# Optimization experiments

Hardware: AMD Instinct MI355X
Metric: run time of the kernel (lower is better)

## Reference

```python
import jax, jax.numpy as jnp
import numpy as np

DIM = 128
HEADS = 4
HEAD_DIM = DIM // HEADS
WIN = 7
DIL = 1
EPS = 1e-5
HIDDEN = 4 * DIM  # mlp_ratio = 4.0
PAD = DIL * (WIN // 2)


def setup_inputs() -> dict:
    key = jax.random.key(0)
    ks = jax.random.split(key, 16)
    s = 0.02
    return {
        "x": jax.random.normal(ks[0], (8, DIM, 256, 256), dtype=jnp.float32),
        "n1_w": jnp.ones((DIM,), jnp.float32),
        "n1_b": jnp.zeros((DIM,), jnp.float32),
        "qkv_w": jax.random.normal(ks[1], (3 * DIM, DIM), jnp.float32) * s,
        "qkv_b": jnp.zeros((3 * DIM,), jnp.float32),
        "proj_w": jax.random.normal(ks[2], (DIM, DIM), jnp.float32) * s,
        "proj_b": jnp.zeros((DIM,), jnp.float32),
        "n2_w": jnp.ones((DIM,), jnp.float32),
        "n2_b": jnp.zeros((DIM,), jnp.float32),
        "mlp_w1": jax.random.normal(ks[3], (HIDDEN, DIM), jnp.float32) * s,
        "mlp_b1": jnp.zeros((HIDDEN,), jnp.float32),
        "mlp_w2": jax.random.normal(ks[4], (DIM, HIDDEN), jnp.float32) * s,
        "mlp_b2": jnp.zeros((DIM,), jnp.float32),
    }


def _channel_ln(x, w, b):
    # LayerNorm over channel axis (axis=1) of NCHW, per spatial location
    mu = jnp.mean(x, axis=1, keepdims=True)
    var = jnp.mean(jnp.square(x - mu), axis=1, keepdims=True)
    xn = (x - mu) * jax.lax.rsqrt(var + EPS)
    return xn * w[None, :, None, None] + b[None, :, None, None]


def _local_attn(x, qkv_w, qkv_b, proj_w, proj_b):
    B, C, H, W = x.shape
    qkv = jnp.einsum("oc,bchw->bohw", qkv_w, x) + qkv_b[None, :, None, None]
    q, k, v = jnp.split(qkv, 3, axis=1)
    q = q.reshape(B, HEADS, HEAD_DIM, H, W) * (HEAD_DIM ** -0.5)
    k = k.reshape(B, HEADS, HEAD_DIM, H, W)
    v = v.reshape(B, HEADS, HEAD_DIM, H, W)
    # boundary_pad='zeros': pad key/value maps with zeros
    pad = [(0, 0), (0, 0), (0, 0), (PAD, PAD), (PAD, PAD)]
    kp = jnp.pad(k, pad)
    vp = jnp.pad(v, pad)
    offsets = [(oi, oj) for oi in range(WIN) for oj in range(WIN)]
    scores = []
    for oi, oj in offsets:  # fixed small window loop (49 iters)
        ks = kp[..., oi * DIL : oi * DIL + H, oj * DIL : oj * DIL + W]
        scores.append(jnp.einsum("bhcij,bhcij->bhij", q, ks))
    scores = jnp.stack(scores, axis=-1)
    attn = jax.nn.softmax(scores, axis=-1)
    out = jnp.zeros_like(v)
    for idx, (oi, oj) in enumerate(offsets):
        vs = vp[..., oi * DIL : oi * DIL + H, oj * DIL : oj * DIL + W]
        out = out + attn[..., idx][:, :, None] * vs
    out = out.reshape(B, C, H, W)
    return jnp.einsum("oc,bchw->bohw", proj_w, out) + proj_b[None, :, None, None]


def _mlp(x, w1, b1, w2, b2):
    h = jnp.einsum("oc,bchw->bohw", w1, x) + b1[None, :, None, None]
    h = jax.nn.gelu(h)
    return jnp.einsum("oc,bchw->bohw", w2, h) + b2[None, :, None, None]


def reference(x, n1_w, n1_b, qkv_w, qkv_b, proj_w, proj_b, n2_w, n2_b, mlp_w1, mlp_b1, mlp_w2, mlp_b2):
    x = x + _local_attn(_channel_ln(x, n1_w, n1_b), qkv_w, qkv_b, proj_w, proj_b)
    x = x + _mlp(_channel_ln(x, n2_w, n2_b), mlp_w1, mlp_b1, mlp_w2, mlp_b2)
    return x
```

## Files before the change

kernel.cpp:

```cpp
#include <hip/hip_runtime.h>
#include <hip/hip_bf16.h>

typedef unsigned short u16;
typedef unsigned int u32;
typedef __attribute__((ext_vector_type(4))) u32 u32x4;
typedef __attribute__((ext_vector_type(2))) u32 u32x2;
typedef __attribute__((ext_vector_type(8))) __bf16 bf16x8;
typedef __attribute__((ext_vector_type(4))) float f32x4;
typedef __attribute__((ext_vector_type(4))) short short4v;

#define HW 65536
#define MFMA32(a, b, c) __builtin_amdgcn_mfma_f32_16x16x32_bf16((a), (b), (c), 0, 0, 0)

__device__ __forceinline__ u16 f2bf(float f){
  union { u32 i; float f; } v; v.f = f;
  u32 r = v.i + 0x7fffu + ((v.i >> 16) & 1u);
  return (u16)(r >> 16);
}
__device__ __forceinline__ u32 pkbf(float a, float b){
  __bf16 lo = (__bf16)a, hi = (__bf16)b;
  u16 ulo = __builtin_bit_cast(u16, lo);
  u16 uhi = __builtin_bit_cast(u16, hi);
  return (u32)ulo | ((u32)uhi << 16);
}
__device__ __forceinline__ float rcpf(float x){
#if __has_builtin(__builtin_amdgcn_rcpf)
  return __builtin_amdgcn_rcpf(x);
#else
  return 1.0f / x;
#endif
}
__device__ __forceinline__ float gelu_tanh(float v){
  float t = v * v;
  float u = fmaf(0.044715f * t, v, v);
  float z = 1.5957691216057308f * u;
  float e = __expf(-z);
  return v * rcpf(1.0f + e);
}

__device__ __forceinline__ f32x4 mfma16bf16(short4v a, short4v b, f32x4 c){
#if __has_builtin(__builtin_amdgcn_mfma_f32_16x16x16bf16_1k)
  return __builtin_amdgcn_mfma_f32_16x16x16bf16_1k(a, b, c, 0, 0, 0);
#else
  f32x4 d;
  asm volatile("v_mfma_f32_16x16x16_bf16 %0, %1, %2, %3"
               : "=v"(d) : "v"(a), "v"(b), "v"(c));
  return d;
#endif
}

__global__ __launch_bounds__(256) void k_pack(
    const float* __restrict__ qkvw, const float* __restrict__ projw,
    const float* __restrict__ w1, const float* __restrict__ w2,
    u16* __restrict__ wf)
{
  int tile = blockIdx.x;
  int t = threadIdx.x;
  int l = t >> 1, half = t & 1;
  if (l >= 64) return;
  int lg = l >> 4;
  if (tile >= 256){
    int ti = tile - 256;
    int hp = ti >> 3, m = ti & 7;
    int row = m * 16 + (l & 15);
    u16 o[4];
    #pragma unroll
    for (int j = 0; j < 4; ++j){
      int s = half * 4 + j;
      int kloc = (s < 4) ? (4 * lg + s) : (16 + 4 * lg + (s - 4));
      o[j] = f2bf(w2[(size_t)row * 512 + hp * 32 + kloc]);
    }
    u32x2 v; v[0] = (u32)o[0] | ((u32)o[1] << 16); v[1] = (u32)o[2] | ((u32)o[3] << 16);
    *(u32x2*)(wf + 131072 + ti * 512 + l * 8 + half * 4) = v;
    return;
  }
  const float* W; int base, ti;
  if (tile < 96)       { W = qkvw; base = 0;     ti = tile; }
  else if (tile < 128) { W = projw; base = 49152; ti = tile - 96; }
  else                 { W = w1;   base = 65536; ti = tile - 128; }
  int mt = ti / 4, kt = ti % 4;
  int r0 = half * 4;
  int m = mt * 16 + (l & 15);
  int kb = kt * 32 + 8 * lg + r0;
  u16 o[4];
  #pragma unroll
  for (int j = 0; j < 4; ++j) o[j] = f2bf(W[(size_t)m * 128 + kb + j]);
  u32x2 v; v[0] = (u32)o[0] | ((u32)o[1] << 16); v[1] = (u32)o[2] | ((u32)o[3] << 16);
  *(u32x2*)(wf + base + ti * 512 + l * 8 + r0) = v;
}

__global__ __launch_bounds__(256, 2) void k_ln_qkv(
    const float* __restrict__ x, const float* __restrict__ n1w,
    const float* __restrict__ n1b, const u16* __restrict__ wfq,
    const float* __restrict__ qkvb, u16* __restrict__ qkvp)
{
  __shared__ __align__(16) char smem[66560];
  float* red  = (float*)(smem + 16384);
  float* mu_s = (float*)(smem + 18432);
  float* rs_s = (float*)(smem + 18688);

  const int t = threadIdx.x;
  const int w = t >> 6, l = t & 63;
  const int P0 = blockIdx.x * 64;
  const int b = P0 >> 16;
  const int pix0 = P0 & 65535;
  const float* xb = x + ((size_t)b * 128) * HW + pix0 + l;

  float xv[32];
  float s = 0.f, s2 = 0.f;
  #pragma unroll
  for (int j = 0; j < 32; ++j){
    float v = xb[(size_t)(w * 32 + j) * HW];
    xv[j] = v; s += v; s2 += v * v;
  }
  red[w * 64 + l] = s;
  red[256 + w * 64 + l] = s2;
  __syncthreads();
  if (t < 64){
    float ss  = red[t] + red[64 + t] + red[128 + t] + red[192 + t];
    float ss2 = red[256 + t] + red[320 + t] + red[384 + t] + red[448 + t];
    float mu = ss * 0.0078125f;
    float var = ss2 * 0.0078125f - mu * mu;
    mu_s[t] = mu; rs_s[t] = rsqrtf(var + 1e-5f);
  }
  __syncthreads();
  {
    float mu = mu_s[l], rs = rs_s[l];
    #pragma unroll
    for (int jj = 0; jj < 4; ++jj){
      int c0 = w * 32 + jj * 8;
      u32x4 pk;
      #pragma unroll
      for (int k2 = 0; k2 < 4; ++k2){
        float v0 = (xv[jj*8 + k2*2    ] - mu) * rs * n1w[c0 + k2*2    ] + n1b[c0 + k2*2    ];
        float v1 = (xv[jj*8 + k2*2 + 1] - mu) * rs * n1w[c0 + k2*2 + 1] + n1b[c0 + k2*2 + 1];
        pk[k2] = pkbf(v0, v1);
      }
      *(u32x4*)(smem + l * 256 + (((w * 4 + jj) ^ (l & 7)) << 4)) = pk;
    }
  }
  __syncthreads();

  const int lg = l >> 4, ln = l & 15;
  const bf16x8* wfrag = (const bf16x8*)wfq;
  f32x4 acc[6][4];
  #pragma unroll
  for (int m = 0; m < 6; ++m)
    #pragma unroll
    for (int n = 0; n < 4; ++n) acc[m][n] = (f32x4)(0.f);
  #pragma unroll
  for (int kt = 0; kt < 4; ++kt){
    bf16x8 a[6], bb[4];
    #pragma unroll
    for (int m = 0; m < 6; ++m) a[m] = wfrag[((w*6 + m)*4 + kt)*64 + l];
    #pragma unroll
    for (int n = 0; n < 4; ++n){
      int p = n * 16 + ln;
      bb[n] = *(const bf16x8*)(smem + p * 256 + ((((kt*4 + lg)) ^ (p & 7)) << 4));
    }
    #pragma unroll
    for (int m = 0; m < 6; ++m)
      #pragma unroll
      for (int n = 0; n < 4; ++n)
        acc[m][n] = MFMA32(a[m], bb[n], acc[m][n]);
  }
  #pragma unroll
  for (int m = 0; m < 6; ++m)
    #pragma unroll
    for (int n = 0; n < 4; ++n){
      int o0 = w * 96 + m * 16 + 4 * lg;
      float qs = (o0 < 128) ? 0.17677669529663687f : 1.0f;
      int p = n * 16 + ln;
      u32x2 v;
      v[0] = pkbf((acc[m][n][0] + qkvb[o0+0]) * qs, (acc[m][n][1] + qkvb[o0+1]) * qs);
      v[1] = pkbf((acc[m][n][2] + qkvb[o0+2]) * qs, (acc[m][n][3] + qkvb[o0+3]) * qs);
      *(u32x2*)(smem + 16384 + p * 784 + o0 * 2) = v;
    }
  __syncthreads();
  for (int i = t; i < 3072; i += 256){
    int p = i / 48, c8 = i - p * 48;
    u32x4 v = *(const u32x4*)(smem + 16384 + p * 784 + c8 * 16);
    int sel = c8 >> 4, hh = (c8 >> 2) & 3, c0 = (c8 & 3) * 8;
    u16* plane = qkvp + (size_t)sel * 67108864ull;
    *(u32x4*)(plane + (((size_t)(b*4 + hh)) * 65536 + pix0 + p) * 32 + c0) = v;
  }
}

__global__ __launch_bounds__(256, 2) void k_attn(
    u16* qbuf, const u16* __restrict__ kbuf, const u16* __restrict__ vbuf)
{
  __shared__ __align__(16) u16 Klds[4 * 512 * 8];
  __shared__ __align__(16) u16 VT[32 * 532 + 16];
  const int t = threadIdx.x;
  const int blk = ((blockIdx.x & 7) << 10) | (blockIdx.x >> 3);
  const int tx16 = blk & 15, ty16 = (blk >> 4) & 15;
  const int h = (blk >> 8) & 3, b = blk >> 10;
  const int y0 = ty16 * 16, x0 = tx16 * 16;
  const int bh = b * 4 + h;
  const u16* kg = kbuf + (size_t)bh * 65536 * 32;
  const u16* vg = vbuf + (size_t)bh * 65536 * 32;

  for (int i = t; i < 2130; i += 256) ((u32x4*)VT)[i] = (u32x4){0u,0u,0u,0u};
  __syncthreads();

  for (int pix = t; pix < 484; pix += 256){
    int yy = pix / 22, xx = pix - yy * 22;
    int gy = y0 + yy - 3, gx = x0 + xx - 3;
    bool ok = (gy >= 0 && gy < 256 && gx >= 0 && gx < 256);
    u32x4 kv[4], vv[4];
    #pragma unroll
    for (int j = 0; j < 4; ++j){ kv[j] = (u32x4){0u,0u,0u,0u}; vv[j] = (u32x4){0u,0u,0u,0u}; }
    if (ok){
      size_t gb = ((size_t)(gy * 256 + gx)) * 32;
      #pragma unroll
      for (int j = 0; j < 4; ++j){
        kv[j] = *(const u32x4*)(kg + gb + j * 8);
        vv[j] = *(const u32x4*)(vg + gb + j * 8);
      }
    }
    #pragma unroll
    for (int j = 0; j < 4; ++j)
      *(u32x4*)(Klds + (j * 512 + pix) * 8) = kv[j];
    int vb = yy * 24 + xx;
    #pragma unroll
    for (int j = 0; j < 4; ++j)
      #pragma unroll
      for (int ww = 0; ww < 4; ++ww){
        int c = j * 8 + ww * 2;
        VT[(c    ) * 532 + vb] = (u16)(vv[j][ww] & 0xffffu);
        VT[(c + 1) * 532 + vb] = (u16)(vv[j][ww] >> 16);
      }
  }
  __syncthreads();

  const int l = t & 63, w = t >> 6;
  const int ln = l & 15, g = l >> 4;

  bool mk[2][4];
  #pragma unroll
  for (int sl = 0; sl < 2; ++sl)
    #pragma unroll
    for (int r = 0; r < 4; ++r)
      mk[sl][r] = ((unsigned)(sl * 16 + g * 4 + r - ln)) <= 6u;

  for (int rt = 0; rt < 4; ++rt){
    int yl = rt * 4 + w;
    int qpix = (y0 + yl) * 256 + x0 + ln;
    u16* qp = qbuf + ((size_t)bh * 65536 + qpix) * 32;
    bf16x8 qf = *(const bf16x8*)(qp + g * 8);

    f32x4 S[7][2];
    #pragma unroll
    for (int oi = 0; oi < 7; ++oi){
      int rowb = (yl + oi) * 22;
      #pragma unroll
      for (int sl = 0; sl < 2; ++sl){
        bf16x8 kf = *(const bf16x8*)(Klds + (g * 512 + rowb + sl * 16 + ln) * 8);
        f32x4 z = (f32x4)(0.f);
        S[oi][sl] = MFMA32(kf, qf, z);
      }
    }
    float m = -3e38f;
    #pragma unroll
    for (int oi = 0; oi < 7; ++oi)
      #pragma unroll
      for (int sl = 0; sl < 2; ++sl)
        #pragma unroll
        for (int r = 0; r < 4; ++r){
          float v = mk[sl][r] ? S[oi][sl][r] : -3e38f;
          S[oi][sl][r] = v;
          m = fmaxf(m, v);
        }
    m = fmaxf(m, __shfl_xor(m, 16));
    m = fmaxf(m, __shfl_xor(m, 32));
    float sum = 0.f;
    #pragma unroll
    for (int oi = 0; oi < 7; ++oi)
      #pragma unroll
      for (int sl = 0; sl < 2; ++sl)
        #pragma unroll
        for (int r = 0; r < 4; ++r){
          float e = __expf(S[oi][sl][r] - m);
          S[oi][sl][r] = e;
          sum += e;
        }
    sum += __shfl_xor(sum, 16);
    sum += __shfl_xor(sum, 32);
    float inv = 1.f / sum;

    short4v P[7][2];
    #pragma unroll
    for (int oi = 0; oi < 7; ++oi)
      #pragma unroll
      for (int sl = 0; sl < 2; ++sl){
        union { u32x2 u; short4v s; } cv;
        cv.u[0] = pkbf(S[oi][sl][0], S[oi][sl][1]);
        cv.u[1] = pkbf(S[oi][sl][2], S[oi][sl][3]);
        P[oi][sl] = cv.s;
      }

    f32x4 O0 = (f32x4)(0.f), O1 = (f32x4)(0.f);
    #pragma unroll
    for (int oi = 0; oi < 7; ++oi){
      int rowE = (yl + oi) * 24;
      #pragma unroll
      for (int sl = 0; sl < 2; ++sl){
        int xb = rowE + sl * 16 + 4 * g;
        short4v v0 = *(const short4v*)(VT + (ln     ) * 532 + xb);
        short4v v1 = *(const short4v*)(VT + (ln + 16) * 532 + xb);
        O0 = mfma16bf16(v0, P[oi][sl], O0);
        O1 = mfma16bf16(v1, P[oi][sl], O1);
      }
    }
    u32x2 o0, o1;
    o0[0] = pkbf(O0[0]*inv, O0[1]*inv);
    o0[1] = pkbf(O0[2]*inv, O0[3]*inv);
    o1[0] = pkbf(O1[0]*inv, O1[1]*inv);
    o1[1] = pkbf(O1[2]*inv, O1[3]*inv);
    *(u32x2*)(qp + 4 * g)      = o0;
    *(u32x2*)(qp + 16 + 4 * g) = o1;
  }
}

__global__ __launch_bounds__(256, 3) void k_proj_mlp(
    const u16* __restrict__ ao, const u16* __restrict__ wfp,
    const float* __restrict__ projb, const float* __restrict__ x,
    const float* __restrict__ n2w, const float* __restrict__ n2b,
    const u16* __restrict__ wf1, const float* __restrict__ b1,
    const u16* __restrict__ wf2, const float* __restrict__ b2,
    float* __restrict__ yout)
{
  __shared__ __align__(16) char smem[32768];
  const int t = threadIdx.x;
  const int w = t >> 6, l = t & 63, lg = l >> 4, ln = l & 15;
  const int P0 = blockIdx.x * 128;
  const int b = P0 >> 16;
  const int pix0 = P0 & 65535;

  auto stage8k = [&](const u16* gsrc, int ldsoff){
    const char* g = (const char*)gsrc;
    int base = w * 2048;
    #pragma unroll
    for (int i = 0; i < 2; ++i){
      int off = base + i * 1024;
      __builtin_amdgcn_global_load_lds(
        (const u32 __attribute__((address_space(1)))*)(g + off + l * 16),
        (u32 __attribute__((address_space(3)))*)(smem + ldsoff + off),
        16, 0, 0);
    }
  };

  stage8k(wfp,          0);
  stage8k(wfp + 4096,   8192);
  stage8k(wfp + 8192,  16384);
  stage8k(wfp + 12288, 24576);

  const int pA = w * 32 + ln;
  const int pB = pA + 16;

  bf16x8 bbA[4], bbB[4];
  #pragma unroll
  for (int kt = 0; kt < 4; ++kt){
    const u16* hb = ao + ((size_t)(b * 4 + kt)) * 2097152ull;
    bbA[kt] = *(const bf16x8*)(hb + (size_t)(pix0 + pA) * 32 + lg * 8);
    bbB[kt] = *(const bf16x8*)(hb + (size_t)(pix0 + pB) * 32 + lg * 8);
  }
  float xrA[8][4], xrB[8][4];
  #pragma unroll
  for (int m = 0; m < 8; ++m){
    int c0 = m * 16 + 4 * lg;
    size_t base = ((size_t)(b * 128 + c0)) * HW + pix0 + pA;
    #pragma unroll
    for (int r = 0; r < 4; ++r){
      xrA[m][r] = x[base + (size_t)r * HW];
      xrB[m][r] = x[base + 16 + (size_t)r * HW];
    }
  }
  __syncthreads();

  f32x4 yvA[8], yvB[8];
  #pragma unroll
  for (int m = 0; m < 8; ++m){ yvA[m] = (f32x4)(0.f); yvB[m] = (f32x4)(0.f); }
  #pragma unroll
  for (int kt = 0; kt < 4; ++kt)
    #pragma unroll
    for (int m = 0; m < 8; ++m){
      int off = (m < 4) ? ((m*4 + kt) << 10) : (16384 + (((m-4)*4 + kt) << 10));
      bf16x8 a = *(const bf16x8*)(smem + off + l * 16);
      yvA[m] = MFMA32(a, bbA[kt], yvA[m]);
      yvB[m] = MFMA32(a, bbB[kt], yvB[m]);
    }
  __syncthreads();
  stage8k(wf1, 0);
  stage8k(wf2, 8192);

  float sA = 0.f, s2A = 0.f, sB = 0.f, s2B = 0.f;
  #pragma unroll
  for (int m = 0; m < 8; ++m){
    int c0 = m * 16 + 4 * lg;
    f32x4 pbv = *(const f32x4*)(projb + c0);
    #pragma unroll
    for (int r = 0; r < 4; ++r){
      float vA = xrA[m][r] + yvA[m][r] + pbv[r];
      float vB = xrB[m][r] + yvB[m][r] + pbv[r];
      yvA[m][r] = vA; yvB[m][r] = vB;
      sA += vA; s2A = fmaf(vA, vA, s2A);
      sB += vB; s2B = fmaf(vB, vB, s2B);
    }
  }
  sA  += __shfl_xor(sA, 16);  sA  += __shfl_xor(sA, 32);
  s2A += __shfl_xor(s2A, 16); s2A += __shfl_xor(s2A, 32);
  sB  += __shfl_xor(sB, 16);  sB  += __shfl_xor(sB, 32);
  s2B += __shfl_xor(s2B, 16); s2B += __shfl_xor(s2B, 32);
  float muA = sA * 0.0078125f;
  float rsA = rsqrtf(s2A * 0.0078125f - muA * muA + 1e-5f);
  float muB = sB * 0.0078125f;
  float rsB = rsqrtf(s2B * 0.0078125f - muB * muB + 1e-5f);

  {
    char* wbase = smem + 16384 + w * 4096;
    #pragma unroll
    for (int m = 0; m < 8; ++m){
      int c0 = m * 16 + 4 * lg;
      f32x4 wv = *(const f32x4*)(n2w + c0);
      f32x4 bv = *(const f32x4*)(n2b + c0);
      int g8 = c0 >> 3;
      u32x2 pk;
      pk[0] = pkbf((yvA[m][0]-muA)*rsA*wv[0]+bv[0], (yvA[m][1]-muA)*rsA*wv[1]+bv[1]);
      pk[1] = pkbf((yvA[m][2]-muA)*rsA*wv[2]+bv[2], (yvA[m][3]-muA)*rsA*wv[3]+bv[3]);
      *(u32x2*)(wbase + ln * 256 + ((g8 ^ (ln & 7)) << 4) + ((lg & 1) << 3)) = pk;
    }
    #pragma unroll
    for (int kt = 0; kt < 4; ++kt)
      bbA[kt] = *(const bf16x8*)(wbase + ln * 256 + (((kt*4 + lg) ^ (ln & 7)) << 4));
    #pragma unroll
    for (int m = 0; m < 8; ++m){
      int c0 = m * 16 + 4 * lg;
      f32x4 wv = *(const f32x4*)(n2w + c0);
      f32x4 bv = *(const f32x4*)(n2b + c0);
      int g8 = c0 >> 3;
      u32x2 pk;
      pk[0] = pkbf((yvB[m][0]-muB)*rsB*wv[0]+bv[0], (yvB[m][1]-muB)*rsB*wv[1]+bv[1]);
      pk[1] = pkbf((yvB[m][2]-muB)*rsB*wv[2]+bv[2], (yvB[m][3]-muB)*rsB*wv[3]+bv[3]);
      *(u32x2*)(wbase + ln * 256 + ((g8 ^ (ln & 7)) << 4) + ((lg & 1) << 3)) = pk;
    }
    #pragma unroll
    for (int kt = 0; kt < 4; ++kt)
      bbB[kt] = *(const bf16x8*)(wbase + ln * 256 + (((kt*4 + lg) ^ (ln & 7)) << 4));
  }

  f32x4 acA[8], acB[8];
  #pragma unroll
  for (int m = 0; m < 8; ++m){
    int c0 = m * 16 + 4 * lg;
    f32x4 b2v = *(const f32x4*)(b2 + c0);
    #pragma unroll
    for (int r = 0; r < 4; ++r){
      acA[m][r] = yvA[m][r] + b2v[r];
      acB[m][r] = yvB[m][r] + b2v[r];
    }
  }
  __syncthreads();

  for (int c = 0; c < 16; ++c){
    const int cur = (c & 1) ? 16384 : 0;
    if (c < 15){
      const int nxt = cur ^ 16384;
      stage8k(wf1 + (c + 1) * 4096, nxt);
      stage8k(wf2 + (c + 1) * 4096, nxt + 8192);
    }
    f32x4 hA[2], hB[2];
    hA[0] = (f32x4)(0.f); hA[1] = (f32x4)(0.f);
    hB[0] = (f32x4)(0.f); hB[1] = (f32x4)(0.f);
    #pragma unroll
    for (int kt = 0; kt < 4; ++kt)
      #pragma unroll
      for (int mt = 0; mt < 2; ++mt){
        bf16x8 a = *(const bf16x8*)(smem + cur + ((mt*4 + kt) << 10) + l * 16);
        hA[mt] = MFMA32(a, bbA[kt], hA[mt]);
        hB[mt] = MFMA32(a, bbB[kt], hB[mt]);
      }
    int hb0 = c * 32 + 4 * lg;
    f32x4 b1a = *(const f32x4*)(b1 + hb0);
    f32x4 b1b = *(const f32x4*)(b1 + hb0 + 16);
    bf16x8 hfA, hfB;
    {
      union { u32x4 u; bf16x8 h; } uu;
      uu.u[0] = pkbf(gelu_tanh(hA[0][0]+b1a[0]), gelu_tanh(hA[0][1]+b1a[1]));
      uu.u[1] = pkbf(gelu_tanh(hA[0][2]+b1a[2]), gelu_tanh(hA[0][3]+b1a[3]));
      uu.u[2] = pkbf(gelu_tanh(hA[1][0]+b1b[0]), gelu_tanh(hA[1][1]+b1b[1]));
      uu.u[3] = pkbf(gelu_tanh(hA[1][2]+b1b[2]), gelu_tanh(hA[1][3]+b1b[3]));
      hfA = uu.h;
      uu.u[0] = pkbf(gelu_tanh(hB[0][0]+b1a[0]), gelu_tanh(hB[0][1]+b1a[1]));
      uu.u[1] = pkbf(gelu_tanh(hB[0][2]+b1a[2]), gelu_tanh(hB[0][3]+b1a[3]));
      uu.u[2] = pkbf(gelu_tanh(hB[1][0]+b1b[0]), gelu_tanh(hB[1][1]+b1b[1]));
      uu.u[3] = pkbf(gelu_tanh(hB[1][2]+b1b[2]), gelu_tanh(hB[1][3]+b1b[3]));
      hfB = uu.h;
    }
    #pragma unroll
    for (int m = 0; m < 8; ++m){
      bf16x8 a = *(const bf16x8*)(smem + cur + 8192 + (m << 10) + l * 16);
      acA[m] = MFMA32(a, hfA, acA[m]);
      acB[m] = MFMA32(a, hfB, acB[m]);
    }
    if (c < 15) __syncthreads();
  }

  #pragma unroll
  for (int m = 0; m < 8; ++m){
    int c0 = m * 16 + 4 * lg;
    size_t base = ((size_t)(b * 128 + c0)) * HW + pix0 + pA;
    #pragma unroll
    for (int r = 0; r < 4; ++r){
      yout[base + (size_t)r * HW]      = acA[m][r];
      yout[base + 16 + (size_t)r * HW] = acB[m][r];
    }
  }
}

extern "C" void kernel_launch(void* const* d_in, const int* in_sizes, int n_in,
                              void* d_out, int out_size, void* d_ws, size_t ws_size,
                              hipStream_t stream)
{
  const float* x    = (const float*)d_in[0];
  const float* n1w  = (const float*)d_in[1];
  const float* n1b  = (const float*)d_in[2];
  const float* qkvw = (const float*)d_in[3];
  const float* qkvb = (const float*)d_in[4];
  const float* pw   = (const float*)d_in[5];
  const float* pb   = (const float*)d_in[6];
  const float* n2w  = (const float*)d_in[7];
  const float* n2b  = (const float*)d_in[8];
  const float* w1   = (const float*)d_in[9];
  const float* b1   = (const float*)d_in[10];
  const float* w2   = (const float*)d_in[11];
  const float* b2   = (const float*)d_in[12];

  u16* qkvp = (u16*)d_ws;
  u16* qbuf = qkvp;
  u16* kbuf = qkvp + 67108864ull;
  u16* vbuf = qkvp + 134217728ull;
  u16* wf   = qkvp + 201326592ull;
  u16* wfq = wf;
  u16* wfp = wf + 49152;
  u16* wf1 = wf + 65536;
  u16* wf2 = wf + 131072;
  float* y = (float*)d_out;

  k_pack<<<384, 256, 0, stream>>>(qkvw, pw, w1, w2, wf);
  k_ln_qkv<<<8192, 256, 0, stream>>>(x, n1w, n1b, wfq, qkvb, qkvp);
  k_attn<<<8192, 256, 0, stream>>>(qbuf, kbuf, vbuf);
  k_proj_mlp<<<4096, 256, 0, stream>>>(qbuf, wfp, pb, x, n2w, n2b, wf1, b1, wf2, b2, y);
}
```

Before: 693.5 us.

## Fold LayerNorm affine into weights, restructure QKV kernel, shrink attention tiles

LayerNorm scale and shift, plus the q scaling, are folded into the packed QKV and MLP1 weights and into precomputed biases inside the pack kernel. This removes per-element affine math and bias lookups from the hot kernels. The LN+QKV kernel is rewritten in the same style as the proj/MLP kernel: 128 pixels per block, shuffle-based reductions, weights staged into LDS with double buffering, and direct output stores. The attention kernel switches to 8-row tiles with smaller LDS so three blocks fit per CU. The cost is more halo loading per pixel in attention, and rounding to bf16 after folding the affine into the weights changes numerics slightly.

Result: faster. 615.9 us (-11.2%).

```diff
diff --git a/kernel.cpp b/kernel.cpp
--- a/kernel.cpp
+++ b/kernel.cpp
@@ -52,10 +52,31 @@
 __global__ __launch_bounds__(256) void k_pack(
     const float* __restrict__ qkvw, const float* __restrict__ projw,
     const float* __restrict__ w1, const float* __restrict__ w2,
+    const float* __restrict__ n1w, const float* __restrict__ n1b,
+    const float* __restrict__ n2w, const float* __restrict__ n2b,
+    const float* __restrict__ qkvb, const float* __restrict__ b1,
     u16* __restrict__ wf)
 {
+  const float S = 0.17677669529663687f;
   int tile = blockIdx.x;
   int t = threadIdx.x;
+  float* bias = (float*)(wf + 196608);
+  if (tile >= 384){
+    if (tile < 386){
+      int o = (tile - 384) * 256 + t;
+      if (o < 384){
+        float s = qkvb[o];
+        for (int c = 0; c < 128; ++c) s = fmaf(qkvw[(size_t)o * 128 + c], n1b[c], s);
+        bias[o] = s * (o < 128 ? S : 1.f);
+      }
+    } else {
+      int h = (tile - 386) * 256 + t;
+      float s = b1[h];
+      for (int c = 0; c < 128; ++c) s = fmaf(w1[(size_t)h * 128 + c], n2b[c], s);
+      bias[384 + h] = s;
+    }
+    return;
+  }
   int l = t >> 1, half = t & 1;
   if (l >= 64) return;
   int lg = l >> 4;
@@ -74,136 +95,159 @@
     *(u32x2*)(wf + 131072 + ti * 512 + l * 8 + half * 4) = v;
     return;
   }
-  const float* W; int base, ti;
-  if (tile < 96)       { W = qkvw; base = 0;     ti = tile; }
-  else if (tile < 128) { W = projw; base = 49152; ti = tile - 96; }
-  else                 { W = w1;   base = 65536; ti = tile - 128; }
+  const float* W; int base, ti; int mode;
+  if (tile < 96)       { W = qkvw; base = 0;     ti = tile;      mode = 0; }
+  else if (tile < 128) { W = projw; base = 49152; ti = tile - 96; mode = 1; }
+  else                 { W = w1;   base = 65536; ti = tile - 128; mode = 2; }
   int mt = ti / 4, kt = ti % 4;
   int r0 = half * 4;
   int m = mt * 16 + (l & 15);
   int kb = kt * 32 + 8 * lg + r0;
   u16 o[4];
   #pragma unroll
-  for (int j = 0; j < 4; ++j) o[j] = f2bf(W[(size_t)m * 128 + kb + j]);
+  for (int j = 0; j < 4; ++j){
+    float wv = W[(size_t)m * 128 + kb + j];
+    if (mode == 0) wv *= n1w[kb + j] * (m < 128 ? S : 1.f);
+    if (mode == 2) wv *= n2w[kb + j];
+    o[j] = f2bf(wv);
+  }
   u32x2 v; v[0] = (u32)o[0] | ((u32)o[1] << 16); v[1] = (u32)o[2] | ((u32)o[3] << 16);
   *(u32x2*)(wf + base + ti * 512 + l * 8 + r0) = v;
 }
 
-__global__ __launch_bounds__(256, 2) void k_ln_qkv(
-    const float* __restrict__ x, const float* __restrict__ n1w,
-    const float* __restrict__ n1b, const u16* __restrict__ wfq,
-    const float* __restrict__ qkvb, u16* __restrict__ qkvp)
+__global__ __launch_bounds__(256, 3) void k_ln_qkv(
+    const float* __restrict__ x, const u16* __restrict__ wfq,
+    const float* __restrict__ bq, u16* __restrict__ qkvp)
 {
-  __shared__ __align__(16) char smem[66560];
-  float* red  = (float*)(smem + 16384);
-  float* mu_s = (float*)(smem + 18432);
-  float* rs_s = (float*)(smem + 18688);
-
+  __shared__ __align__(16) char smem[32768];
   const int t = threadIdx.x;
-  const int w = t >> 6, l = t & 63;
-  const int P0 = blockIdx.x * 64;
+  const int w = t >> 6, l = t & 63, lg = l >> 4, ln = l & 15;
+  const int P0 = blockIdx.x * 128;
   const int b = P0 >> 16;
   const int pix0 = P0 & 65535;
-  const float* xb = x + ((size_t)b * 128) * HW + pix0 + l;
-
-  float xv[32];
-  float s = 0.f, s2 = 0.f;
-  #pragma unroll
-  for (int j = 0; j < 32; ++j){
-    float v = xb[(size_t)(w * 32 + j) * HW];
-    xv[j] = v; s += v; s2 += v * v;
-  }
-  red[w * 64 + l] = s;
-  red[256 + w * 64 + l] = s2;
+
+  auto stage8k = [&](const u16* gsrc, int ldsoff){
+    const char* g = (const char*)gsrc;
+    int base = w * 2048;
+    #pragma unroll
+    for (int i = 0; i < 2; ++i){
+      int off = base + i * 1024;
+      __builtin_amdgcn_global_load_lds(
+        (const u32 __attribute__((address_space(1)))*)(g + off + l * 16),
+        (u32 __attribute__((address_space(3)))*)(smem + ldsoff + off),
+        16, 0, 0);
+    }
+  };
+
+  stage8k(wfq, 0);
+  stage8k(wfq + 4096, 8192);
+
+  const int pA = w * 32 + ln, pB = pA + 16;
+
+  float xA[8][4], xB[8][4];
+  float sA = 0.f, s2A = 0.f, sB = 0.f, s2B = 0.f;
+  #pragma unroll
+  for (int m = 0; m < 8; ++m){
+    int c0 = m * 16 + 4 * lg;
+    size_t base = ((size_t)(b * 128 + c0)) * HW + pix0 + pA;
+    #pragma unroll
+    for (int r = 0; r < 4; ++r){
+      float vA = x[base + (size_t)r * HW];
+      float vB = x[base + 16 + (size_t)r * HW];
+      xA[m][r] = vA; xB[m][r] = vB;
+      sA += vA; s2A = fmaf(vA, vA, s2A);
+      sB += vB; s2B = fmaf(vB, vB, s2B);
+    }
+  }
+  sA  += __shfl_xor(sA, 16);  sA  += __shfl_xor(sA, 32);
+  s2A += __shfl_xor(s2A, 16); s2A += __shfl_xor(s2A, 32);
+  sB  += __shfl_xor(sB, 16);  sB  += __shfl_xor(sB, 32);
+  s2B += __shfl_xor(s2B, 16); s2B += __shfl_xor(s2B, 32);
+  float muA = sA * 0.0078125f;
+  float rsA = rsqrtf(s2A * 0.0078125f - muA * muA + 1e-5f);
+  float muB = sB * 0.0078125f;
+  float rsB = rsqrtf(s2B * 0.0078125f - muB * muB + 1e-5f);
+
+  bf16x8 bbA[4], bbB[4];
+  {
+    char* wbase = smem + 16384 + w * 4096;
+    #pragma unroll
+    for (int m = 0; m < 8; ++m){
+      int g8 = 2 * m + (lg >> 1);
+      u32x2 pk;
+      pk[0] = pkbf((xA[m][0]-muA)*rsA, (xA[m][1]-muA)*rsA);
+      pk[1] = pkbf((xA[m][2]-muA)*rsA, (xA[m][3]-muA)*rsA);
+      *(u32x2*)(wbase + ln * 256 + ((g8 ^ (ln & 7)) << 4) + ((lg & 1) << 3)) = pk;
+    }
+    #pragma unroll
+    for (int kt = 0; kt < 4; ++kt)
+      bbA[kt] = *(const bf16x8*)(wbase + ln * 256 + (((kt*4 + lg) ^ (ln & 7)) << 4));
+    #pragma unroll
+    for (int m = 0; m < 8; ++m){
+      int g8 = 2 * m + (lg >> 1);
+      u32x2 pk;
+      pk[0] = pkbf((xB[m][0]-muB)*rsB, (xB[m][1]-muB)*rsB);
+      pk[1] = pkbf((xB[m][2]-muB)*rsB, (xB[m][3]-muB)*rsB);
+      *(u32x2*)(wbase + ln * 256 + ((g8 ^ (ln & 7)) << 4) + ((lg & 1) << 3)) = pk;
+    }
+    #pragma unroll
+    for (int kt = 0; kt < 4; ++kt)
+      bbB[kt] = *(const bf16x8*)(wbase + ln * 256 + (((kt*4 + lg) ^ (ln & 7)) << 4));
+  }
   __syncthreads();
-  if (t < 64){
-    float ss  = red[t] + red[64 + t] + red[128 + t] + red[192 + t];
-    float ss2 = red[256 + t] + red[320 + t] + red[384 + t] + red[448 + t];
-    float mu = ss * 0.0078125f;
-    float var = ss2 * 0.0078125f - mu * mu;
-    mu_s[t] = mu; rs_s[t] = rsqrtf(var + 1e-5f);
-  }
-  __syncthreads();
-  {
-    float mu = mu_s[l], rs = rs_s[l];
-    #pragma unroll
-    for (int jj = 0; jj < 4; ++jj){
-      int c0 = w * 32 + jj * 8;
-      u32x4 pk;
-      #pragma unroll
-      for (int k2 = 0; k2 < 4; ++k2){
-        float v0 = (xv[jj*8 + k2*2    ] - mu) * rs * n1w[c0 + k2*2    ] + n1b[c0 + k2*2    ];
-        float v1 = (xv[jj*8 + k2*2 + 1] - mu) * rs * n1w[c0 + k2*2 + 1] + n1b[c0 + k2*2 + 1];
-        pk[k2] = pkbf(v0, v1);
-      }
-      *(u32x4*)(smem + l * 256 + (((w * 4 + jj) ^ (l & 7)) << 4)) = pk;
-    }
-  }
-  __syncthreads();
-
-  const int lg = l >> 4, ln = l & 15;
-  const bf16x8* wfrag = (const bf16x8*)wfq;
-  f32x4 acc[6][4];
-  #pragma unroll
-  for (int m = 0; m < 6; ++m)
-    #pragma unroll
-    for (int n = 0; n < 4; ++n) acc[m][n] = (f32x4)(0.f);
-  #pragma unroll
-  for (int kt = 0; kt < 4; ++kt){
-    bf16x8 a[6], bb[4];
-    #pragma unroll
-    for (int m = 0; m < 6; ++m) a[m] = wfrag[((w*6 + m)*4 + kt)*64 + l];
-    #pragma unroll
-    for (int n = 0; n < 4; ++n){
-      int p = n * 16 + ln;
-      bb[n] = *(const bf16x8*)(smem + p * 256 + ((((kt*4 + lg)) ^ (p & 7)) << 4));
-    }
-    #pragma unroll
-    for (int m = 0; m < 6; ++m)
-      #pragma unroll
-      for (int n = 0; n < 4; ++n)
-        acc[m][n] = MFMA32(a[m], bb[n], acc[m][n]);
-  }
-  #pragma unroll
-  for (int m = 0; m < 6; ++m)
-    #pragma unroll
-    for (int n = 0; n < 4; ++n){
-      int o0 = w * 96 + m * 16 + 4 * lg;
-      float qs = (o0 < 128) ? 0.17677669529663687f : 1.0f;
-      int p = n * 16 + ln;
-      u32x2 v;
-      v[0] = pkbf((acc[m][n][0] + qkvb[o0+0]) * qs, (acc[m][n][1] + qkvb[o0+1]) * qs);
-      v[1] = pkbf((acc[m][n][2] + qkvb[o0+2]) * qs, (acc[m][n][3] + qkvb[o0+3]) * qs);
-      *(u32x2*)(smem + 16384 + p * 784 + o0 * 2) = v;
-    }
-  __syncthreads();
-  for (int i = t; i < 3072; i += 256){
-    int p = i / 48, c8 = i - p * 48;
-    u32x4 v = *(const u32x4*)(smem + 16384 + p * 784 + c8 * 16);
-    int sel = c8 >> 4, hh = (c8 >> 2) & 3, c0 = (c8 & 3) * 8;
-    u16* plane = qkvp + (size_t)sel * 67108864ull;
-    *(u32x4*)(plane + (((size_t)(b*4 + hh)) * 65536 + pix0 + p) * 32 + c0) = v;
-  }
-}
-
-__global__ __launch_bounds__(256, 2) void k_attn(
+
+  for (int c = 0; c < 6; ++c){
+    const int cur = (c & 1) ? 16384 : 0;
+    if (c < 5){
+      const int nxt = cur ^ 16384;
+      stage8k(wfq + (c + 1) * 8192, nxt);
+      stage8k(wfq + (c + 1) * 8192 + 4096, nxt + 8192);
+    }
+    #pragma unroll
+    for (int mt = 0; mt < 4; ++mt){
+      f32x4 dA = (f32x4)(0.f), dB = (f32x4)(0.f);
+      #pragma unroll
+      for (int kt = 0; kt < 4; ++kt){
+        bf16x8 a = *(const bf16x8*)(smem + cur + ((mt*4 + kt) << 10) + l * 16);
+        dA = MFMA32(a, bbA[kt], dA);
+        dB = MFMA32(a, bbB[kt], dB);
+      }
+      int o0 = c * 64 + mt * 16 + 4 * lg;
+      f32x4 bqv = *(const f32x4*)(bq + o0);
+      u32x2 vA, vB;
+      vA[0] = pkbf(dA[0]+bqv[0], dA[1]+bqv[1]);
+      vA[1] = pkbf(dA[2]+bqv[2], dA[3]+bqv[3]);
+      vB[0] = pkbf(dB[0]+bqv[0], dB[1]+bqv[1]);
+      vB[1] = pkbf(dB[2]+bqv[2], dB[3]+bqv[3]);
+      u16* plane = qkvp + (size_t)(o0 >> 7) * 67108864ull;
+      int hh = (o0 >> 5) & 3;
+      int sub = o0 & 31;
+      size_t pbase = ((size_t)(b * 4 + hh)) * 65536 + pix0;
+      *(u32x2*)(plane + (pbase + pA) * 32 + sub) = vA;
+      *(u32x2*)(plane + (pbase + pB) * 32 + sub) = vB;
+    }
+    if (c < 5) __syncthreads();
+  }
+}
+
+__global__ __launch_bounds__(256, 3) void k_attn(
     u16* qbuf, const u16* __restrict__ kbuf, const u16* __restrict__ vbuf)
 {
-  __shared__ __align__(16) u16 Klds[4 * 512 * 8];
-  __shared__ __align__(16) u16 VT[32 * 532 + 16];
+  __shared__ __align__(16) u16 Klds[4 * 320 * 8];
+  __shared__ __align__(16) u16 VT[32 * 344 + 8];
   const int t = threadIdx.x;
-  const int blk = ((blockIdx.x & 7) << 10) | (blockIdx.x >> 3);
-  const int tx16 = blk & 15, ty16 = (blk >> 4) & 15;
-  const int h = (blk >> 8) & 3, b = blk >> 10;
-  const int y0 = ty16 * 16, x0 = tx16 * 16;
+  const int blk = ((blockIdx.x & 7) << 11) | (blockIdx.x >> 3);
+  const int tx16 = blk & 15, ty = (blk >> 4) & 31;
+  const int h = (blk >> 9) & 3, b = blk >> 11;
+  const int y0 = ty * 8, x0 = tx16 * 16;
   const int bh = b * 4 + h;
   const u16* kg = kbuf + (size_t)bh * 65536 * 32;
   const u16* vg = vbuf + (size_t)bh * 65536 * 32;
 
-  for (int i = t; i < 2130; i += 256) ((u32x4*)VT)[i] = (u32x4){0u,0u,0u,0u};
+  for (int i = t; i < 1377; i += 256) ((u32x4*)VT)[i] = (u32x4){0u,0u,0u,0u};
   __syncthreads();
 
-  for (int pix = t; pix < 484; pix += 256){
+  for (int pix = t; pix < 308; pix += 256){
     int yy = pix / 22, xx = pix - yy * 22;
     int gy = y0 + yy - 3, gx = x0 + xx - 3;
     bool ok = (gy >= 0 && gy < 256 && gx >= 0 && gx < 256);
@@ -220,15 +264,15 @@
     }
     #pragma unroll
     for (int j = 0; j < 4; ++j)
-      *(u32x4*)(Klds + (j * 512 + pix) * 8) = kv[j];
+      *(u32x4*)(Klds + (j * 320 + pix) * 8) = kv[j];
     int vb = yy * 24 + xx;
     #pragma unroll
     for (int j = 0; j < 4; ++j)
       #pragma unroll
       for (int ww = 0; ww < 4; ++ww){
         int c = j * 8 + ww * 2;
-        VT[(c    ) * 532 + vb] = (u16)(vv[j][ww] & 0xffffu);
-        VT[(c + 1) * 532 + vb] = (u16)(vv[j][ww] >> 16);
+        VT[(c    ) * 344 + vb] = (u16)(vv[j][ww] & 0xffffu);
+        VT[(c + 1) * 344 + vb] = (u16)(vv[j][ww] >> 16);
       }
   }
   __syncthreads();
@@ -243,7 +287,7 @@
     for (int r = 0; r < 4; ++r)
       mk[sl][r] = ((unsigned)(sl * 16 + g * 4 + r - ln)) <= 6u;
 
-  for (int rt = 0; rt < 4; ++rt){
+  for (int rt = 0; rt < 2; ++rt){
     int yl = rt * 4 + w;
     int qpix = (y0 + yl) * 256 + x0 + ln;
     u16* qp = qbuf + ((size_t)bh * 65536 + qpix) * 32;
@@ -255,7 +299,7 @@
       int rowb = (yl + oi) * 22;
       #pragma unroll
       for (int sl = 0; sl < 2; ++sl){
-        bf16x8 kf = *(const bf16x8*)(Klds + (g * 512 + rowb + sl * 16 + ln) * 8);
+        bf16x8 kf = *(const bf16x8*)(Klds + (g * 320 + rowb + sl * 16 + ln) * 8);
         f32x4 z = (f32x4)(0.f);
         S[oi][sl] = MFMA32(kf, qf, z);
       }
@@ -306,8 +350,8 @@
       #pragma unroll
       for (int sl = 0; sl < 2; ++sl){
         int xb = rowE + sl * 16 + 4 * g;
-        short4v v0 = *(const short4v*)(VT + (ln     ) * 532 + xb);
-        short4v v1 = *(const short4v*)(VT + (ln + 16) * 532 + xb);
+        short4v v0 = *(const short4v*)(VT + (ln     ) * 344 + xb);
+        short4v v1 = *(const short4v*)(VT + (ln + 16) * 344 + xb);
         O0 = mfma16bf16(v0, P[oi][sl], O0);
         O1 = mfma16bf16(v1, P[oi][sl], O1);
       }
@@ -325,8 +369,7 @@
 __global__ __launch_bounds__(256, 3) void k_proj_mlp(
     const u16* __restrict__ ao, const u16* __restrict__ wfp,
     const float* __restrict__ projb, const float* __restrict__ x,
-    const float* __restrict__ n2w, const float* __restrict__ n2b,
-    const u16* __restrict__ wf1, const float* __restrict__ b1,
+    const u16* __restrict__ wf1, const float* __restrict__ b1p,
     const u16* __restrict__ wf2, const float* __restrict__ b2,
     float* __restrict__ yout)
 {
@@ -421,13 +464,10 @@
     char* wbase = smem + 16384 + w * 4096;
     #pragma unroll
     for (int m = 0; m < 8; ++m){
-      int c0 = m * 16 + 4 * lg;
-      f32x4 wv = *(const f32x4*)(n2w + c0);
-      f32x4 bv = *(const f32x4*)(n2b + c0);
-      int g8 = c0 >> 3;
+      int g8 = 2 * m + (lg >> 1);
       u32x2 pk;
-      pk[0] = pkbf((yvA[m][0]-muA)*rsA*wv[0]+bv[0], (yvA[m][1]-muA)*rsA*wv[1]+bv[1]);
-      pk[1] = pkbf((yvA[m][2]-muA)*rsA*wv[2]+bv[2], (yvA[m][3]-muA)*rsA*wv[3]+bv[3]);
+      pk[0] = pkbf((yvA[m][0]-muA)*rsA, (yvA[m][1]-muA)*rsA);
+      pk[1] = pkbf((yvA[m][2]-muA)*rsA, (yvA[m][3]-muA)*rsA);
       *(u32x2*)(wbase + ln * 256 + ((g8 ^ (ln & 7)) << 4) + ((lg & 1) << 3)) = pk;
     }
     #pragma unroll
@@ -435,13 +475,10 @@
       bbA[kt] = *(const bf16x8*)(wbase + ln * 256 + (((kt*4 + lg) ^ (ln & 7)) << 4));
     #pragma unroll
     for (int m = 0; m < 8; ++m){
-      int c0 = m * 16 + 4 * lg;
-      f32x4 wv = *(const f32x4*)(n2w + c0);
-      f32x4 bv = *(const f32x4*)(n2b + c0);
-      int g8 = c0 >> 3;
+      int g8 = 2 * m + (lg >> 1);
       u32x2 pk;
-      pk[0] = pkbf((yvB[m][0]-muB)*rsB*wv[0]+bv[0], (yvB[m][1]-muB)*rsB*wv[1]+bv[1]);
-      pk[1] = pkbf((yvB[m][2]-muB)*rsB*wv[2]+bv[2], (yvB[m][3]-muB)*rsB*wv[3]+bv[3]);
+      pk[0] = pkbf((yvB[m][0]-muB)*rsB, (yvB[m][1]-muB)*rsB);
+      pk[1] = pkbf((yvB[m][2]-muB)*rsB, (yvB[m][3]-muB)*rsB);
       *(u32x2*)(wbase + ln * 256 + ((g8 ^ (ln & 7)) << 4) + ((lg & 1) << 3)) = pk;
     }
     #pragma unroll
@@ -481,8 +518,8 @@
         hB[mt] = MFMA32(a, bbB[kt], hB[mt]);
       }
     int hb0 = c * 32 + 4 * lg;
-    f32x4 b1a = *(const f32x4*)(b1 + hb0);
-    f32x4 b1b = *(const f32x4*)(b1 + hb0 + 16);
+    f32x4 b1a = *(const f32x4*)(b1p + hb0);
+    f32x4 b1b = *(const f32x4*)(b1p + hb0 + 16);
     bf16x8 hfA, hfB;
     {
       union { u32x4 u; bf16x8 h; } uu;
@@ -545,10 +582,11 @@
   u16* wfp = wf + 49152;
   u16* wf1 = wf + 65536;
   u16* wf2 = wf + 131072;
+  float* bias = (float*)(wf + 196608);
   float* y = (float*)d_out;
 
-  k_pack<<<384, 256, 0, stream>>>(qkvw, pw, w1, w2, wf);
-  k_ln_qkv<<<8192, 256, 0, stream>>>(x, n1w, n1b, wfq, qkvb, qkvp);
-  k_attn<<<8192, 256, 0, stream>>>(qbuf, kbuf, vbuf);
-  k_proj_mlp<<<4096, 256, 0, stream>>>(qbuf, wfp, pb, x, n2w, n2b, wf1, b1, wf2, b2, y);
-}
+  k_pack<<<388, 256, 0, stream>>>(qkvw, pw, w1, w2, n1w, n1b, n2w, n2b, qkvb, b1, wf);
+  k_ln_qkv<<<4096, 256, 0, stream>>>(x, wfq, bias, qkvp);
+  k_attn<<<16384, 256, 0, stream>>>(qbuf, kbuf, vbuf);
+  k_proj_mlp<<<4096, 256, 0, stream>>>(qbuf, wfp, pb, x, wf1, bias + 384, wf2, b2, y);
+}
```
